# Performance work log

Hardware: AMD Instinct MI355X
Metric: run time of the kernel (lower is better)

Reference implementation:

```python
import math
import jax, jax.numpy as jnp
import numpy as np

D_MODEL = 1024
NHEAD = 16
NUM_TEMP = 4
HEAD = D_MODEL // NHEAD          # 64
DIM = HEAD // NUM_TEMP           # 16
SCALE = math.sqrt(HEAD)
B, L = 2, 2048


def _make_freq():
    # freq = 10000^(-arange(0,dim,2)/dim), repeat_interleave(2) -> length DIM
    f = np.power(10000.0, -np.arange(0, DIM, 2) / DIM)
    return jnp.asarray(np.repeat(f, 2), dtype=jnp.float32)  # (DIM,)


def setup_inputs() -> dict:
    key = jax.random.key(0)
    ks = jax.random.split(key, 8)
    s = 0.02
    return {
        "data": jax.random.normal(ks[0], (B, L, D_MODEL), jnp.float32),
        "temporal": jax.random.uniform(ks[1], (B, L, NUM_TEMP), jnp.float32),
        "mask": jnp.zeros((L, L), jnp.float32),
        "Wq": jax.random.normal(ks[2], (D_MODEL, D_MODEL), jnp.float32) * s,
        "bq": jnp.zeros((D_MODEL,), jnp.float32),
        "Wk": jax.random.normal(ks[3], (D_MODEL, D_MODEL), jnp.float32) * s,
        "bk": jnp.zeros((D_MODEL,), jnp.float32),
        "Wv": jax.random.normal(ks[4], (D_MODEL, D_MODEL), jnp.float32) * s,
        "bv": jnp.zeros((D_MODEL,), jnp.float32),
    }


def _rotate_half_pairs(x):
    # [-x2, x1, -x4, x3, ...] along last dim
    stacked = jnp.stack([-x[..., 1::2], x[..., 0::2]], axis=-1)
    return stacked.reshape(x.shape)


def _apply_rotary(x, sine, cosine):
    # x: (B,L,H,HEAD); sine/cosine: (B,L,HEAD)
    return x * cosine[:, :, None, :] + _rotate_half_pairs(x) * sine[:, :, None, :]


def reference(data, temporal, mask, Wq, bq, Wk, bk, Wv, bv):
    freq = _make_freq()  # (DIM,)
    b, l, _ = data.shape
    q = (data @ Wq + bq).reshape(b, l, NHEAD, HEAD)
    k = (data @ Wk + bk).reshape(b, l, NHEAD, HEAD)
    v = (data @ Wv + bv).reshape(b, l, NHEAD, HEAD)
    # per-temporal-column frequencies: (B,L,T,DIM) -> (B,L,HEAD)
    freqs = (temporal[..., None] * freq).reshape(b, l, HEAD)
    cosine = jnp.cos(freqs)
    sine = jnp.sin(freqs)
    rq = _apply_rotary(q, sine, cosine)
    rk = _apply_rotary(k, sine, cosine)
    logits = jnp.einsum("bqhs,bkhs->bhqk", rq, rk) / SCALE + mask
    weights = jax.nn.softmax(logits, axis=-1)  # dropout is identity at eval
    context = jnp.einsum("bhqk,bkhs->bqhs", weights, v)
    return context.reshape(b, l, D_MODEL)
```

## Files before the change

kernel.cpp:

```cpp
#include <hip/hip_runtime.h>
#include <hip/hip_bf16.h>

#define LSEQ 2048
#define DM   1024
#define NH   16

typedef __attribute__((ext_vector_type(8)))  short bf16x8;
typedef __attribute__((ext_vector_type(8)))  unsigned short u16x8;
typedef __attribute__((ext_vector_type(4)))  float f32x4;
typedef __attribute__((ext_vector_type(16))) float f32x16;
typedef __attribute__((ext_vector_type(4)))  unsigned int u32x4;

#define LOG2E 1.4426950408889634f
#define C1SC  0.18033688011112042f

static __device__ __forceinline__ float exp2fast(float x) {
  return __builtin_amdgcn_exp2f(x);
}

static __device__ __forceinline__ unsigned short f2bf(float f) {
  unsigned int u = __float_as_uint(f);
  u += 0x7FFFu + ((u >> 16) & 1u);
  return (unsigned short)(u >> 16);
}

static __device__ __forceinline__ float bf2f(unsigned short u) {
  return __uint_as_float(((unsigned int)u) << 16);
}

static __device__ __forceinline__ unsigned pk2(float a, float b) {
  __hip_bfloat162 t = __float22bfloat162_rn(make_float2(a, b));
  return *reinterpret_cast<unsigned*>(&t);
}

static __device__ __forceinline__ bf16x8 mkfrag(int hi, float p0, float p1,
                                                float p2, float p3, float p4,
                                                float p5, float p6, float p7) {
  unsigned w0 = pk2(p0, p1), w1 = pk2(p2, p3);
  unsigned w2 = pk2(p4, p5), w3 = pk2(p6, p7);
  unsigned s0 = hi ? w0 : w2, s1 = hi ? w1 : w3;
  unsigned t0 = __shfl_xor(s0, 32, 64);
  unsigned t1 = __shfl_xor(s1, 32, 64);
  u32x4 f;
  f[0] = hi ? t0 : w0;
  f[1] = hi ? t1 : w1;
  f[2] = hi ? w2 : t0;
  f[3] = hi ? w3 : t1;
  return __builtin_bit_cast(bf16x8, f);
}

static __device__ __forceinline__ void gld_lds16(const unsigned short* g, unsigned short* l) {
  __builtin_amdgcn_global_load_lds(
      (const __attribute__((address_space(1))) unsigned int*)g,
      (__attribute__((address_space(3))) unsigned int*)l, 16, 0, 0);
}

__global__ void k_convert_data(const float* __restrict__ src,
                               unsigned short* __restrict__ dst, int n4) {
  int i = blockIdx.x * 256 + threadIdx.x;
  if (i >= n4) return;
  float4 v = reinterpret_cast<const float4*>(src)[i];
  ushort4 o;
  o.x = f2bf(v.x); o.y = f2bf(v.y); o.z = f2bf(v.z); o.w = f2bf(v.w);
  reinterpret_cast<ushort4*>(dst)[i] = o;
}

__global__ void k_transpose_w(const float* __restrict__ Wq,
                              const float* __restrict__ Wk,
                              const float* __restrict__ Wv,
                              unsigned short* __restrict__ Wt) {
  __shared__ unsigned short tile[64][65];
  const float* W = (blockIdx.z == 0) ? Wq : (blockIdx.z == 1) ? Wk : Wv;
  int n0 = blockIdx.x * 64, k0 = blockIdx.y * 64;
  int t = threadIdx.x;
  int c = t & 63, r0 = t >> 6;
  for (int i = 0; i < 16; ++i) {
    int r = r0 + i * 4;
    tile[r][c] = f2bf(W[(size_t)(k0 + r) * DM + n0 + c]);
  }
  __syncthreads();
  size_t nbase = (size_t)blockIdx.z * DM + n0;
  for (int i = 0; i < 16; ++i) {
    int n = r0 + i * 4;
    Wt[(nbase + n) * DM + k0 + c] = tile[c][n];
  }
}

__global__ void k_maskT(const float* __restrict__ mask,
                        unsigned short* __restrict__ maskT) {
  __shared__ float tile[64][65];
  int q0 = blockIdx.x * 64, kv0 = blockIdx.y * 64;
  int t = threadIdx.x;
  int c = t & 63, r0 = t >> 6;
  for (int i = 0; i < 16; ++i) {
    int r = r0 + i * 4;
    tile[r][c] = mask[(size_t)(q0 + r) * LSEQ + kv0 + c];
  }
  __syncthreads();
  for (int i = 0; i < 16; ++i) {
    int n = r0 + i * 4;
    maskT[(size_t)(kv0 + n) * LSEQ + q0 + c] = f2bf(tile[c][n] * LOG2E);
  }
}

__global__ __launch_bounds__(256) void k_qkv_gemm(
    const unsigned short* __restrict__ A, const unsigned short* __restrict__ Bt,
    const float* __restrict__ bq, const float* __restrict__ bk,
    const float* __restrict__ bv, const float* __restrict__ temporal,
    unsigned short* __restrict__ qbuf, unsigned short* __restrict__ kbuf,
    unsigned short* __restrict__ vtbuf) {
  __shared__ unsigned short As[128 * 32];
  __shared__ unsigned short Bs[128 * 32];
  __shared__ unsigned short otile[128 * 136];
  const int tid = threadIdx.x;
  const int lane = tid & 63, wid = tid >> 6;
  const int wm = wid >> 1, wn = wid & 1;
  const int lr = lane & 15, lg = lane >> 4;

  const int bid = blockIdx.x;
  const int xcd = bid & 7, rr = bid >> 3;
  const int mblk = xcd * 4 + (rr / 24);
  const int nblk = rr % 24;
  const int m0 = mblk * 128;
  const int n0 = nblk * 128;

  f32x4 acc[4][4] = {};

  const int e0 = tid * 8;
  const int e1 = (256 + tid) * 8;
  const int ra0 = e0 >> 5, ca0 = e0 & 31;
  const int ra1 = e1 >> 5, ca1 = e1 & 31;
  unsigned short* lA0 = As + wid * 512;
  unsigned short* lA1 = As + 2048 + wid * 512;
  unsigned short* lB0 = Bs + wid * 512;
  unsigned short* lB1 = Bs + 2048 + wid * 512;

  for (int k0 = 0; k0 < DM; k0 += 32) {
    __syncthreads();
    gld_lds16(A + (size_t)(m0 + ra0) * DM + k0 + ca0, lA0);
    gld_lds16(A + (size_t)(m0 + ra1) * DM + k0 + ca1, lA1);
    gld_lds16(Bt + (size_t)(n0 + ra0) * DM + k0 + ca0, lB0);
    gld_lds16(Bt + (size_t)(n0 + ra1) * DM + k0 + ca1, lB1);
    __syncthreads();
    bf16x8 af[4], bfv[4];
    for (int mi = 0; mi < 4; ++mi)
      af[mi] = *reinterpret_cast<const bf16x8*>(As + (wm * 64 + mi * 16 + lr) * 32 + lg * 8);
    for (int ni = 0; ni < 4; ++ni)
      bfv[ni] = *reinterpret_cast<const bf16x8*>(Bs + (wn * 64 + ni * 16 + lr) * 32 + lg * 8);
    for (int mi = 0; mi < 4; ++mi)
      for (int ni = 0; ni < 4; ++ni)
        acc[mi][ni] = __builtin_amdgcn_mfma_f32_16x16x32_bf16(af[mi], bfv[ni], acc[mi][ni], 0, 0, 0);
  }

  const int mat = n0 >> 10;
  const int c0 = n0 & 1023;
  const int bb = m0 >> 11;
  const int mloc = m0 & 2047;

  for (int mi = 0; mi < 4; ++mi) {
    const int rrel_base = wm * 64 + mi * 16 + lg * 4;
    for (int ni = 0; ni < 4; ++ni) {
      const int crel = wn * 64 + ni * 16 + lr;
      const int c = (c0 + crel);
      const int d = c & 63;
      const float bias = (mat == 0 ? bq : mat == 1 ? bk : bv)[c];
      f32x4 v = acc[mi][ni];
      if (mat < 2) {
        const int jj = d & 15, tt = d >> 4;
        const float fr = __expf(-(float)(jj & 14) * 0.5756462732485115f);
        const float sign = (d & 1) ? 1.f : -1.f;
        for (int j = 0; j < 4; ++j) {
          const int rrel = rrel_base + j;
          const float x = v[j] + bias;
          const float part = __shfl_xor(x, 1, 64);
          const int lqs = mloc + rrel;
          const float fq = temporal[((size_t)bb * LSEQ + lqs) * 4 + tt] * fr;
          float sn, cs;
          __sincosf(fq, &sn, &cs);
          otile[rrel * 136 + crel] = f2bf(x * cs + sign * part * sn);
        }
      } else {
        for (int j = 0; j < 4; ++j) {
          const int rrel = rrel_base + j;
          otile[crel * 136 + rrel] = f2bf(v[j] + bias);
        }
      }
    }
  }
  __syncthreads();

  for (int i = 0; i < 2; ++i) {
    const int h = (c0 >> 6) + i;
    const size_t bh = (size_t)(bb * NH + h);
    if (mat == 0) {
      const size_t base = (bh * LSEQ + mloc) * 64;
#pragma unroll
      for (int kk2 = 0; kk2 < 4; ++kk2) {
        const int e = kk2 * 2048 + tid * 8;
        const int r = e >> 6, d = e & 63;
        *reinterpret_cast<u16x8*>(qbuf + base + e) =
            *reinterpret_cast<const u16x8*>(otile + r * 136 + i * 64 + d);
      }
    } else if (mat == 1) {
      const size_t base = bh * 131072 + (size_t)(mloc >> 5) * 2048;
#pragma unroll
      for (int kk2 = 0; kk2 < 4; ++kk2) {
        const int e = kk2 * 2048 + tid * 8;
        const int r = kk2 * 32 + ((tid >> 1) & 31);
        const int d = ((tid >> 6) & 3) * 16 + (tid & 1) * 8;
        *reinterpret_cast<u16x8*>(kbuf + base + e) =
            *reinterpret_cast<const u16x8*>(otile + r * 136 + i * 64 + d);
      }
    } else {
      const size_t base = bh * 131072 + (size_t)(mloc >> 4) * 1024;
#pragma unroll
      for (int kk2 = 0; kk2 < 4; ++kk2) {
        const int e = kk2 * 2048 + tid * 8;
        const int d = ((tid >> 6) & 1) * 32 + ((tid >> 1) & 31);
        const int r = (kk2 * 2 + (tid >> 7)) * 16 + (tid & 1) * 8;
        *reinterpret_cast<u16x8*>(vtbuf + base + e) =
            *reinterpret_cast<const u16x8*>(otile + (i * 64 + d) * 136 + r);
      }
    }
  }
}

__global__ __launch_bounds__(256) void k_attn(
    const unsigned short* __restrict__ qbuf, const unsigned short* __restrict__ kbuf,
    const unsigned short* __restrict__ vtbuf, const unsigned short* __restrict__ maskT,
    float* __restrict__ out) {
  __shared__ float otile[4][64][33];
  const int tid = threadIdx.x, lane = tid & 63, wid = tid >> 6;
  const int lq = lane & 31, hi = lane >> 5;
  const int bh = blockIdx.y;
  const int q0 = blockIdx.x * 128 + wid * 32;
  const int qg = q0 + lq;
  const size_t bhL = (size_t)bh * LSEQ;
  const unsigned short* kb = kbuf + (size_t)bh * 131072;
  const unsigned short* vb = vtbuf + (size_t)bh * 131072;

  bf16x8 qf[4];
#pragma unroll
  for (int c = 0; c < 4; ++c)
    qf[c] = *reinterpret_cast<const bf16x8*>(qbuf + (bhL + qg) * 64 + c * 16 + hi * 8);

  f32x16 o0 = {}, o1 = {};
  float m2 = -1e30f, l_run = 0.f;

  for (int kv0 = 0; kv0 < LSEQ; kv0 += 64) {
    float mk0[16], mk1[16];
#pragma unroll
    for (int r = 0; r < 16; ++r) {
      const int cr = (r & 3) + 8 * (r >> 2) + 4 * hi;
      mk0[r] = bf2f(maskT[(size_t)(kv0 + cr) * LSEQ + qg]);
      mk1[r] = bf2f(maskT[(size_t)(kv0 + 32 + cr) * LSEQ + qg]);
    }

    const unsigned short* kch = kb + (size_t)(kv0 >> 5) * 2048;
    f32x16 s0 = {}, s1 = {};
#pragma unroll
    for (int c = 0; c < 4; ++c) {
      bf16x8 k0 = *reinterpret_cast<const bf16x8*>(kch + c * 512 + lq * 16 + hi * 8);
      bf16x8 k1 = *reinterpret_cast<const bf16x8*>(kch + 2048 + c * 512 + lq * 16 + hi * 8);
      s0 = __builtin_amdgcn_mfma_f32_32x32x16_bf16(k0, qf[c], s0, 0, 0, 0);
      s1 = __builtin_amdgcn_mfma_f32_32x32x16_bf16(k1, qf[c], s1, 0, 0, 0);
    }

#pragma unroll
    for (int r = 0; r < 16; ++r) {
      s0[r] = s0[r] * C1SC + mk0[r];
      s1[r] = s1[r] * C1SC + mk1[r];
    }

    float loc = fmaxf(s0[0], s1[0]);
#pragma unroll
    for (int r = 1; r < 16; ++r) loc = fmaxf(loc, fmaxf(s0[r], s1[r]));
    loc = fmaxf(loc, __shfl_xor(loc, 32, 64));

    if (!__all(loc <= m2)) {
      const float mn = fmaxf(m2, loc);
      const float al = exp2fast(m2 - mn);
      l_run *= al;
#pragma unroll
      for (int r = 0; r < 16; ++r) { o0[r] *= al; o1[r] *= al; }
      m2 = mn;
    }

    float rs = 0.f;
#pragma unroll
    for (int r = 0; r < 16; ++r) {
      s0[r] = exp2fast(s0[r] - m2); rs += s0[r];
      s1[r] = exp2fast(s1[r] - m2); rs += s1[r];
    }
    rs += __shfl_xor(rs, 32, 64);
    l_run += rs;

    bf16x8 pf0 = mkfrag(hi, s0[0], s0[1], s0[2], s0[3], s0[4], s0[5], s0[6], s0[7]);
    bf16x8 pf1 = mkfrag(hi, s0[8], s0[9], s0[10], s0[11], s0[12], s0[13], s0[14], s0[15]);
    bf16x8 pf2 = mkfrag(hi, s1[0], s1[1], s1[2], s1[3], s1[4], s1[5], s1[6], s1[7]);
    bf16x8 pf3 = mkfrag(hi, s1[8], s1[9], s1[10], s1[11], s1[12], s1[13], s1[14], s1[15]);

    const unsigned short* vch = vb + (size_t)(kv0 >> 4) * 1024;
#pragma unroll
    for (int ks = 0; ks < 4; ++ks) {
      bf16x8 pf = (ks == 0) ? pf0 : (ks == 1) ? pf1 : (ks == 2) ? pf2 : pf3;
      bf16x8 v0 = *reinterpret_cast<const bf16x8*>(vch + ks * 1024 + lq * 16 + hi * 8);
      bf16x8 v1 = *reinterpret_cast<const bf16x8*>(vch + ks * 1024 + 512 + lq * 16 + hi * 8);
      o0 = __builtin_amdgcn_mfma_f32_32x32x16_bf16(v0, pf, o0, 0, 0, 0);
      o1 = __builtin_amdgcn_mfma_f32_32x32x16_bf16(v1, pf, o1, 0, 0, 0);
    }
  }

  const float inv = 1.f / l_run;
#pragma unroll
  for (int r = 0; r < 16; ++r) {
    const int d = (r & 3) + 8 * (r >> 2) + 4 * hi;
    otile[wid][d][lq] = o0[r] * inv;
    otile[wid][32 + d][lq] = o1[r] * inv;
  }
  __syncthreads();
  const int b = bh >> 4, h = bh & 15;
#pragma unroll
  for (int i = 0; i < 8; ++i) {
    const int u = i * 64 + lane;
    const int q = u >> 4, c4 = u & 15;
    float4 w;
    w.x = otile[wid][c4 * 4 + 0][q];
    w.y = otile[wid][c4 * 4 + 1][q];
    w.z = otile[wid][c4 * 4 + 2][q];
    w.w = otile[wid][c4 * 4 + 3][q];
    *reinterpret_cast<float4*>(out + ((size_t)(b * LSEQ + q0 + q)) * DM + h * 64 + c4 * 4) = w;
  }
}

extern "C" void kernel_launch(void* const* d_in, const int* in_sizes, int n_in,
                              void* d_out, int out_size, void* d_ws, size_t ws_size,
                              hipStream_t stream) {
  const float* data     = (const float*)d_in[0];
  const float* temporal = (const float*)d_in[1];
  const float* mask     = (const float*)d_in[2];
  const float* Wq       = (const float*)d_in[3];
  const float* bq       = (const float*)d_in[4];
  const float* Wk       = (const float*)d_in[5];
  const float* bk       = (const float*)d_in[6];
  const float* Wv       = (const float*)d_in[7];
  const float* bv       = (const float*)d_in[8];
  float* out = (float*)d_out;

  char* ws = (char*)d_ws;
  unsigned short* data_bf = (unsigned short*)(ws);
  unsigned short* wt      = (unsigned short*)(ws + (size_t)8  * 1048576);
  unsigned short* qbuf    = (unsigned short*)(ws + (size_t)14 * 1048576);
  unsigned short* kbuf    = (unsigned short*)(ws + (size_t)22 * 1048576);
  unsigned short* vtbuf   = (unsigned short*)(ws + (size_t)30 * 1048576);
  unsigned short* maskT   = data_bf;

  hipLaunchKernelGGL(k_convert_data, dim3(4096), dim3(256), 0, stream,
                     data, data_bf, (2 * LSEQ * DM) / 4);
  hipLaunchKernelGGL(k_transpose_w, dim3(16, 16, 3), dim3(256), 0, stream,
                     Wq, Wk, Wv, wt);
  hipLaunchKernelGGL(k_qkv_gemm, dim3(768), dim3(256), 0, stream,
                     data_bf, wt, bq, bk, bv, temporal, qbuf, kbuf, vtbuf);
  hipLaunchKernelGGL(k_maskT, dim3(32, 32), dim3(256), 0, stream,
                     mask, maskT);
  hipLaunchKernelGGL(k_attn, dim3(16, 32), dim3(256), 0, stream,
                     qbuf, kbuf, vtbuf, maskT, out);
}
```

Before: 158.1 us.

## Pre-swizzle mask into MFMA fragment layout, fold scale into Q, defer rescaling

Rewrites the mask preprocessing kernel to store the bf16 mask in a per-lane contiguous layout that matches the attention kernel's accumulator fragments. The attention kernel can then load it with two 16-byte loads per tile and use it directly as the MFMA accumulator initialiser, instead of issuing 32 scattered 2-byte loads. The softmax scale is folded into Q in the projection epilogue, which drops a multiply-add per score. It also adds a lazy max-rescale threshold and tree-style max/sum reductions. The deferred rescale lets exponents reach up to 2^8 before rescaling, which slightly risks bf16 precision loss in P.

```diff
diff --git a/kernel.cpp b/kernel.cpp
--- a/kernel.cpp
+++ b/kernel.cpp
@@ -13,6 +13,7 @@
 
 #define LOG2E 1.4426950408889634f
 #define C1SC  0.18033688011112042f
+#define DEFER_THR 8.0f
 
 static __device__ __forceinline__ float exp2fast(float x) {
   return __builtin_amdgcn_exp2f(x);
@@ -24,13 +25,23 @@
   return (unsigned short)(u >> 16);
 }
 
-static __device__ __forceinline__ float bf2f(unsigned short u) {
-  return __uint_as_float(((unsigned int)u) << 16);
-}
-
 static __device__ __forceinline__ unsigned pk2(float a, float b) {
   __hip_bfloat162 t = __float22bfloat162_rn(make_float2(a, b));
   return *reinterpret_cast<unsigned*>(&t);
+}
+
+static __device__ __forceinline__ f32x16 unpack16(u16x8 a, u16x8 b) {
+  const u32x4 ua = __builtin_bit_cast(u32x4, a);
+  const u32x4 ub = __builtin_bit_cast(u32x4, b);
+  f32x16 r;
+#pragma unroll
+  for (int i = 0; i < 4; ++i) {
+    r[2 * i]     = __uint_as_float(ua[i] << 16);
+    r[2 * i + 1] = __uint_as_float(ua[i] & 0xFFFF0000u);
+    r[8 + 2 * i]     = __uint_as_float(ub[i] << 16);
+    r[8 + 2 * i + 1] = __uint_as_float(ub[i] & 0xFFFF0000u);
+  }
+  return r;
 }
 
 static __device__ __forceinline__ bf16x8 mkfrag(int hi, float p0, float p1,
@@ -86,8 +97,8 @@
   }
 }
 
-__global__ void k_maskT(const float* __restrict__ mask,
-                        unsigned short* __restrict__ maskT) {
+__global__ void k_maskC(const float* __restrict__ mask,
+                        unsigned short* __restrict__ maskCb) {
   __shared__ float tile[64][65];
   int q0 = blockIdx.x * 64, kv0 = blockIdx.y * 64;
   int t = threadIdx.x;
@@ -97,10 +108,22 @@
     tile[r][c] = mask[(size_t)(q0 + r) * LSEQ + kv0 + c];
   }
   __syncthreads();
-  for (int i = 0; i < 16; ++i) {
-    int n = r0 + i * 4;
-    maskT[(size_t)(kv0 + n) * LSEQ + q0 + c] = f2bf(tile[c][n] * LOG2E);
-  }
+  const int q = t & 63, slot = t >> 6;
+  const int tt = slot >> 1, hh = slot & 1;
+  u16x8 va, vb;
+#pragma unroll
+  for (int r = 0; r < 8; ++r) {
+    const int kvloc = 32 * tt + 4 * hh + (r & 3) + 8 * (r >> 2);
+    va[r] = f2bf(tile[q][kvloc] * LOG2E);
+  }
+#pragma unroll
+  for (int r = 8; r < 16; ++r) {
+    const int kvloc = 32 * tt + 4 * hh + (r & 3) + 8 * (r >> 2);
+    vb[r - 8] = f2bf(tile[q][kvloc] * LOG2E);
+  }
+  unsigned short* dst = maskCb + ((size_t)((kv0 >> 6) * 4 + slot) * 2048 + q0 + q) * 16;
+  *reinterpret_cast<u16x8*>(dst) = va;
+  *reinterpret_cast<u16x8*>(dst + 8) = vb;
 }
 
 __global__ __launch_bounds__(256) void k_qkv_gemm(
@@ -156,6 +179,7 @@
   const int c0 = n0 & 1023;
   const int bb = m0 >> 11;
   const int mloc = m0 & 2047;
+  const float qscale = (mat == 0) ? C1SC : 1.f;
 
   for (int mi = 0; mi < 4; ++mi) {
     const int rrel_base = wm * 64 + mi * 16 + lg * 4;
@@ -177,7 +201,7 @@
           const float fq = temporal[((size_t)bb * LSEQ + lqs) * 4 + tt] * fr;
           float sn, cs;
           __sincosf(fq, &sn, &cs);
-          otile[rrel * 136 + crel] = f2bf(x * cs + sign * part * sn);
+          otile[rrel * 136 + crel] = f2bf((x * cs + sign * part * sn) * qscale);
         }
       } else {
         for (int j = 0; j < 4; ++j) {
@@ -227,7 +251,7 @@
 
 __global__ __launch_bounds__(256) void k_attn(
     const unsigned short* __restrict__ qbuf, const unsigned short* __restrict__ kbuf,
-    const unsigned short* __restrict__ vtbuf, const unsigned short* __restrict__ maskT,
+    const unsigned short* __restrict__ vtbuf, const unsigned short* __restrict__ maskCb,
     float* __restrict__ out) {
   __shared__ float otile[4][64][33];
   const int tid = threadIdx.x, lane = tid & 63, wid = tid >> 6;
@@ -238,6 +262,7 @@
   const size_t bhL = (size_t)bh * LSEQ;
   const unsigned short* kb = kbuf + (size_t)bh * 131072;
   const unsigned short* vb = vtbuf + (size_t)bh * 131072;
+  const unsigned short* mb = maskCb + ((size_t)hi * 2048 + qg) * 16;
 
   bf16x8 qf[4];
 #pragma unroll
@@ -248,16 +273,13 @@
   float m2 = -1e30f, l_run = 0.f;
 
   for (int kv0 = 0; kv0 < LSEQ; kv0 += 64) {
-    float mk0[16], mk1[16];
-#pragma unroll
-    for (int r = 0; r < 16; ++r) {
-      const int cr = (r & 3) + 8 * (r >> 2) + 4 * hi;
-      mk0[r] = bf2f(maskT[(size_t)(kv0 + cr) * LSEQ + qg]);
-      mk1[r] = bf2f(maskT[(size_t)(kv0 + 32 + cr) * LSEQ + qg]);
-    }
+    const unsigned short* mt = mb + (size_t)(kv0 >> 6) * (4 * 2048 * 16);
+    f32x16 s0 = unpack16(*reinterpret_cast<const u16x8*>(mt),
+                         *reinterpret_cast<const u16x8*>(mt + 8));
+    f32x16 s1 = unpack16(*reinterpret_cast<const u16x8*>(mt + 2 * 2048 * 16),
+                         *reinterpret_cast<const u16x8*>(mt + 2 * 2048 * 16 + 8));
 
     const unsigned short* kch = kb + (size_t)(kv0 >> 5) * 2048;
-    f32x16 s0 = {}, s1 = {};
 #pragma unroll
     for (int c = 0; c < 4; ++c) {
       bf16x8 k0 = *reinterpret_cast<const bf16x8*>(kch + c * 512 + lq * 16 + hi * 8);
@@ -266,18 +288,15 @@
       s1 = __builtin_amdgcn_mfma_f32_32x32x16_bf16(k1, qf[c], s1, 0, 0, 0);
     }
 
-#pragma unroll
-    for (int r = 0; r < 16; ++r) {
-      s0[r] = s0[r] * C1SC + mk0[r];
-      s1[r] = s1[r] * C1SC + mk1[r];
-    }
-
-    float loc = fmaxf(s0[0], s1[0]);
-#pragma unroll
-    for (int r = 1; r < 16; ++r) loc = fmaxf(loc, fmaxf(s0[r], s1[r]));
+    float t0[8];
+#pragma unroll
+    for (int r = 0; r < 8; ++r) t0[r] = fmaxf(fmaxf(s0[r], s0[r + 8]), fmaxf(s1[r], s1[r + 8]));
+#pragma unroll
+    for (int r = 0; r < 4; ++r) t0[r] = fmaxf(t0[r], t0[r + 4]);
+    float loc = fmaxf(fmaxf(t0[0], t0[1]), fmaxf(t0[2], t0[3]));
     loc = fmaxf(loc, __shfl_xor(loc, 32, 64));
 
-    if (!__all(loc <= m2)) {
+    if (!__all(loc <= m2 + DEFER_THR)) {
       const float mn = fmaxf(m2, loc);
       const float al = exp2fast(m2 - mn);
       l_run *= al;
@@ -286,12 +305,22 @@
       m2 = mn;
     }
 
-    float rs = 0.f;
-#pragma unroll
-    for (int r = 0; r < 16; ++r) {
-      s0[r] = exp2fast(s0[r] - m2); rs += s0[r];
-      s1[r] = exp2fast(s1[r] - m2); rs += s1[r];
-    }
+    float rs0 = 0.f, rs1 = 0.f, rs2 = 0.f, rs3 = 0.f;
+#pragma unroll
+    for (int r = 0; r < 4; ++r) {
+      s0[r] = exp2fast(s0[r] - m2);      rs0 += s0[r];
+      s0[r + 4] = exp2fast(s0[r + 4] - m2);  rs1 += s0[r + 4];
+      s0[r + 8] = exp2fast(s0[r + 8] - m2);  rs2 += s0[r + 8];
+      s0[r + 12] = exp2fast(s0[r + 12] - m2); rs3 += s0[r + 12];
+    }
+#pragma unroll
+    for (int r = 0; r < 4; ++r) {
+      s1[r] = exp2fast(s1[r] - m2);      rs0 += s1[r];
+      s1[r + 4] = exp2fast(s1[r + 4] - m2);  rs1 += s1[r + 4];
+      s1[r + 8] = exp2fast(s1[r + 8] - m2);  rs2 += s1[r + 8];
+      s1[r + 12] = exp2fast(s1[r + 12] - m2); rs3 += s1[r + 12];
+    }
+    float rs = (rs0 + rs1) + (rs2 + rs3);
     rs += __shfl_xor(rs, 32, 64);
     l_run += rs;
 
@@ -353,7 +382,7 @@
   unsigned short* qbuf    = (unsigned short*)(ws + (size_t)14 * 1048576);
   unsigned short* kbuf    = (unsigned short*)(ws + (size_t)22 * 1048576);
   unsigned short* vtbuf   = (unsigned short*)(ws + (size_t)30 * 1048576);
-  unsigned short* maskT   = data_bf;
+  unsigned short* maskCb  = data_bf;
 
   hipLaunchKernelGGL(k_convert_data, dim3(4096), dim3(256), 0, stream,
                      data, data_bf, (2 * LSEQ * DM) / 4);
@@ -361,8 +390,8 @@
                      Wq, Wk, Wv, wt);
   hipLaunchKernelGGL(k_qkv_gemm, dim3(768), dim3(256), 0, stream,
                      data_bf, wt, bq, bk, bv, temporal, qbuf, kbuf, vtbuf);
-  hipLaunchKernelGGL(k_maskT, dim3(32, 32), dim3(256), 0, stream,
-                     mask, maskT);
+  hipLaunchKernelGGL(k_maskC, dim3(32, 32), dim3(256), 0, stream,
+                     mask, maskCb);
   hipLaunchKernelGGL(k_attn, dim3(16, 32), dim3(256), 0, stream,
-                     qbuf, kbuf, vtbuf, maskT, out);
-}
+                     qbuf, kbuf, vtbuf, maskCb, out);
+}
```

Measured after the change: 138.4 us. -12.4%, faster.
